# Kernel optimization log

Measured on AMD Instinct MI355X. Metric: run time of the kernel, lower is better.

The kernel has to match this reference:

```python
import jax, jax.numpy as jnp
import numpy as np

B, S, D, H = 4, 2048, 1024, 16
DK = D // H
THETA = 10000.0


def apply_rope(x, pos, theta):
    # x: [B, H, S, DK], pos: [S] int
    d = x.shape[-1]
    inv_freq = theta ** (-jnp.arange(0, d, 2, dtype=jnp.float32) / d)  # [d/2]
    ang = pos.astype(jnp.float32)[:, None] * inv_freq[None, :]          # [S, d/2]
    cos, sin = jnp.cos(ang), jnp.sin(ang)
    x1 = x[..., 0::2]
    x2 = x[..., 1::2]
    r1 = x1 * cos - x2 * sin
    r2 = x1 * sin + x2 * cos
    return jnp.stack([r1, r2], axis=-1).reshape(x.shape)


def setup_inputs() -> dict:
    key = jax.random.key(0)
    ks = jax.random.split(key, 5)
    scale = 1.0 / np.sqrt(D)
    x = jax.random.normal(ks[0], (B, S, D), dtype=jnp.float32)
    Wq = jax.random.normal(ks[1], (D, D), dtype=jnp.float32) * scale
    Wk = jax.random.normal(ks[2], (D, D), dtype=jnp.float32) * scale
    Wv = jax.random.normal(ks[3], (D, D), dtype=jnp.float32) * scale
    Wo = jax.random.normal(ks[4], (D, D), dtype=jnp.float32) * scale
    token_positions = jnp.arange(S, dtype=jnp.int32)
    return {"x": x, "token_positions": token_positions,
            "Wq": Wq, "Wk": Wk, "Wv": Wv, "Wo": Wo}


def reference(x, token_positions, Wq, Wk, Wv, Wo):
    b, s, d = x.shape
    # Linear (no bias), weight stored [out, in]: y = x @ W.T
    q = (x @ Wq.T).reshape(b, s, H, DK).transpose(0, 2, 1, 3)  # [B,H,S,DK]
    k = (x @ Wk.T).reshape(b, s, H, DK).transpose(0, 2, 1, 3)
    v = (x @ Wv.T).reshape(b, s, H, DK).transpose(0, 2, 1, 3)
    q = apply_rope(q, token_positions, THETA)
    k = apply_rope(k, token_positions, THETA)
    scores = jnp.einsum('bhqd,bhkd->bhqk', q, k) / jnp.sqrt(jnp.float32(DK))
    causal = jnp.tril(jnp.ones((s, s), dtype=bool))
    scores = jnp.where(causal, scores, -jnp.inf)
    attn = jax.nn.softmax(scores, axis=-1)
    out = jnp.einsum('bhqk,bhkd->bhqd', attn, v)
    out = out.transpose(0, 2, 1, 3).reshape(b, s, d)
    return out @ Wo.T
```

## Files before the change

### kernel.cpp

```cpp
#include <hip/hip_runtime.h>

typedef unsigned short u16;
typedef __bf16 bf16x8 __attribute__((ext_vector_type(8)));
typedef float f32x4 __attribute__((ext_vector_type(4)));
typedef u16 u16x8 __attribute__((ext_vector_type(8)));
typedef u16 u16x4 __attribute__((ext_vector_type(4)));
typedef short s16x4 __attribute__((ext_vector_type(4)));

union V8 { u16x8 u; bf16x8 b; };
union V4 { u16x4 u; s16x4 s; unsigned w[2]; };

#define NB 4
#define NS 2048
#define ND 1024
#define NH 16
#define NDK 64
#define LP 80
#define CP 136
#define QSCL 0.18033688011112042f
#define FMAX 20.0f

__device__ __forceinline__ u16 f2bf(float f) {
  union { float f; unsigned u; } v; v.f = f;
  return (u16)((v.u + 0x7fffu + ((v.u >> 16) & 1u)) >> 16);
}

__device__ __forceinline__ unsigned pk2bf(float a, float b) {
#if __has_builtin(__builtin_amdgcn_cvt_pk_bf16_f32)
  auto v = __builtin_amdgcn_cvt_pk_bf16_f32(a, b);
  unsigned r; __builtin_memcpy(&r, &v, 4);
  return r;
#else
  return (unsigned)f2bf(a) | ((unsigned)f2bf(b) << 16);
#endif
}

__device__ __forceinline__ float fexp2(float x) {
#if __has_builtin(__builtin_amdgcn_exp2f)
  return __builtin_amdgcn_exp2f(x);
#else
  return exp2f(x);
#endif
}

__device__ __forceinline__ bf16x8 lds_frag(const u16* p) {
  V8 t; t.u = *(const u16x8*)p; return t.b;
}

__global__ __launch_bounds__(256) void cvt_bf16(const float* __restrict__ s,
                                                u16* __restrict__ d, int n) {
  const int i = (blockIdx.x * 256 + threadIdx.x) * 8;
  if (i >= n) return;
  const f32x4 lo = *(const f32x4*)(s + i);
  const f32x4 hi = *(const f32x4*)(s + i + 4);
  union { unsigned w[4]; u16x8 v; } o;
  o.w[0] = pk2bf(lo[0], lo[1]);
  o.w[1] = pk2bf(lo[2], lo[3]);
  o.w[2] = pk2bf(hi[0], hi[1]);
  o.w[3] = pk2bf(hi[2], hi[3]);
  *(u16x8*)(d + i) = o.v;
}

__global__ __launch_bounds__(256) void cvt_w4(const float* __restrict__ w0,
                                              const float* __restrict__ w1,
                                              const float* __restrict__ w2,
                                              const float* __restrict__ w3,
                                              u16* __restrict__ d) {
  const float* s = (blockIdx.y == 0) ? w0 : (blockIdx.y == 1) ? w1
                 : (blockIdx.y == 2) ? w2 : w3;
  const int i = (blockIdx.x * 256 + threadIdx.x) * 8;
  const f32x4 lo = *(const f32x4*)(s + i);
  const f32x4 hi = *(const f32x4*)(s + i + 4);
  union { unsigned w[4]; u16x8 v; } o;
  o.w[0] = pk2bf(lo[0], lo[1]);
  o.w[1] = pk2bf(lo[2], lo[3]);
  o.w[2] = pk2bf(hi[0], hi[1]);
  o.w[3] = pk2bf(hi[2], hi[3]);
  *(u16x8*)(d + (size_t)blockIdx.y * ND * ND + i) = o.v;
}

__global__ __launch_bounds__(256) void gemm_qkv(
    const u16* __restrict__ X, const u16* __restrict__ W0,
    const u16* __restrict__ W1, const u16* __restrict__ W2,
    void* __restrict__ O0, void* __restrict__ O1, void* __restrict__ O2,
    const int* __restrict__ tokpos, int modebase) {
  __shared__ u16 smem[2 * 128 * LP];
  u16* ldsA = smem;
  u16* ldsB = smem + 128 * LP;
  const int tid = threadIdx.x;
  const int lane = tid & 63;
  const int w = tid >> 6;
  const int quad = lane >> 4;
  const int l15 = lane & 15;
  const int z = blockIdx.z;
  const u16* Wp = (z == 0) ? W0 : (z == 1) ? W1 : W2;
  void* Op = (z == 0) ? O0 : (z == 1) ? O1 : O2;
  const int mode = modebase + z;
  const int m0 = blockIdx.x * 128;
  const int n0 = blockIdx.y * 128;
  const int wm = (w >> 1) * 64;
  const int wn = (w & 1) * 64;

  const int srow = tid >> 3;
  const int scol = (tid & 7) * 8;
  const u16* Ag = X + (size_t)(m0 + srow) * ND + scol;
  const u16* Bg = Wp + (size_t)(n0 + srow) * ND + scol;

  f32x4 acc[4][4];
  const f32x4 z4 = {0.f, 0.f, 0.f, 0.f};
  for (int i = 0; i < 4; i++)
    for (int j = 0; j < 4; j++) acc[i][j] = z4;

  for (int k0 = 0; k0 < ND; k0 += 64) {
    u16x8 ar[4], br[4];
    for (int r = 0; r < 4; r++) {
      ar[r] = *(const u16x8*)(Ag + (size_t)r * 32 * ND + k0);
      br[r] = *(const u16x8*)(Bg + (size_t)r * 32 * ND + k0);
    }
    __syncthreads();
    for (int r = 0; r < 4; r++) {
      *(u16x8*)&ldsA[(r * 32 + srow) * LP + scol] = ar[r];
      *(u16x8*)&ldsB[(r * 32 + srow) * LP + scol] = br[r];
    }
    __syncthreads();
    for (int kk = 0; kk < 2; kk++) {
      bf16x8 af[4], bfr[4];
      for (int mt = 0; mt < 4; mt++)
        af[mt] = lds_frag(&ldsA[(wm + mt * 16 + l15) * LP + (kk * 4 + quad) * 8]);
      for (int nt = 0; nt < 4; nt++)
        bfr[nt] = lds_frag(&ldsB[(wn + nt * 16 + l15) * LP + (kk * 4 + quad) * 8]);
      for (int mt = 0; mt < 4; mt++)
        for (int nt = 0; nt < 4; nt++)
          acc[mt][nt] = __builtin_amdgcn_mfma_f32_16x16x32_bf16(
              af[mt], bfr[nt], acc[mt][nt], 0, 0, 0);
    }
  }
  __syncthreads();

  if (mode < 2) {
    u16* cb = smem;
    for (int nt = 0; nt < 4; nt++) {
      const int n_g = n0 + wn + nt * 16 + l15;
      const int dk = n_g & 63;
      const float sgn = (dk & 1) ? 1.f : -1.f;
      const float inv_freq = __expf(-(float)(dk >> 1) * 0.28782313662425572f);
      for (int mt = 0; mt < 4; mt++) {
        const int mrow = wm + mt * 16 + quad * 4;
        for (int r = 0; r < 4; r++) {
          const int m_g = m0 + mrow + r;
          float v = acc[mt][nt][r];
          const int s_i = m_g & (NS - 1);
          const float pos = (float)tokpos[s_i];
          const float partner = __shfl_xor(v, 1);
          float sn, cs;
          __sincosf(pos * inv_freq, &sn, &cs);
          v = v * cs + partner * sn * sgn;
          if (mode == 0) v *= QSCL;
          cb[(mrow + r) * CP + wn + nt * 16 + l15] = f2bf(v);
        }
      }
    }
    __syncthreads();
    const int c = (tid & 15) * 8;
    const int h = (n0 + c) >> 6;
    const int dk0 = (n0 + c) & 63;
    for (int p = 0; p < 8; p++) {
      const int row = p * 16 + (tid >> 4);
      const int m_g = m0 + row;
      const int b = m_g >> 11;
      const int s_i = m_g & (NS - 1);
      *(u16x8*)&((u16*)Op)[(size_t)(((b * NH) + h) * NS + s_i) * NDK + dk0] =
          *(const u16x8*)&cb[row * CP + c];
    }
  } else if (mode == 2) {
    u16* cbT = smem;
    for (int nt = 0; nt < 4; nt++)
      for (int mt = 0; mt < 4; mt++)
        for (int r = 0; r < 4; r++)
          cbT[(wn + nt * 16 + l15) * CP + wm + mt * 16 + quad * 4 + r] =
              f2bf(acc[mt][nt][r]);
    __syncthreads();
    const int b = m0 >> 11;
    const int s0 = m0 & (NS - 1);
    const int col = (tid & 15) * 8;
    for (int p = 0; p < 8; p++) {
      const int row = p * 16 + (tid >> 4);
      const int dkg = n0 + row;
      const int h = dkg >> 6;
      *(u16x8*)&((u16*)Op)[(size_t)(((b * NH) + h) * NDK + (dkg & 63)) * NS +
                           s0 + col] = *(const u16x8*)&cbT[row * CP + col];
    }
  } else {
    for (int nt = 0; nt < 4; nt++) {
      const int n_g = n0 + wn + nt * 16 + l15;
      for (int mt = 0; mt < 4; mt++) {
        const int mb = m0 + wm + mt * 16 + quad * 4;
        for (int r = 0; r < 4; r++)
          ((float*)Op)[(size_t)(mb + r) * ND + n_g] = acc[mt][nt][r];
      }
    }
  }
}

__global__ __launch_bounds__(512, 2) void attn(const u16* __restrict__ Q,
                                               const u16* __restrict__ Kc,
                                               const u16* __restrict__ Vt,
                                               u16* __restrict__ AO,
                                               unsigned* __restrict__ ctr) {
  __shared__ u16 smem[2 * 64 * LP];
  u16* kt = smem;
  u16* vt = smem + 64 * LP;
  __shared__ unsigned s_item;
  const int tid = threadIdx.x;
  const int lane = tid & 63;
  const int w = tid >> 6;
  const int quad = lane >> 4;
  const int l15 = lane & 15;

  if (tid == 0) s_item = atomicAdd(ctr, 1u) & 1023u;
  __syncthreads();
  const unsigned item = s_item;
  const int bh = (int)(item >> 4);
  const int jj = (int)(item & 15u);
  const int qt = (jj & 1) ? (jj >> 1) : (15 - (jj >> 1));
  const int q0 = qt * 128;
  const int qg = q0 + w * 16 + l15;
  const int qmin = q0 + w * 16;

  const u16* Qb = Q + (size_t)bh * NS * NDK + (size_t)qg * NDK + quad * 8;
  const bf16x8 qf0 = lds_frag(Qb);
  const bf16x8 qf1 = lds_frag(Qb + 32);

  int koff[2][4];
#pragma unroll
  for (int kk = 0; kk < 2; kk++)
#pragma unroll
    for (int nt = 0; nt < 4; nt++) {
      const int row = nt * 16 + l15;
      koff[kk][nt] = row * LP + (((kk * 4 + quad) ^ (row & 7)) * 8);
    }
  int voff[4][4];
#pragma unroll
  for (int dt = 0; dt < 4; dt++) {
    const int dk = dt * 16 + l15;
    const int xr = dk & 7;
#pragma unroll
    for (int nt = 0; nt < 4; nt++) {
      const int chunk = 2 * nt + (quad >> 1);
      voff[dt][nt] = dk * LP + ((chunk ^ xr) * 8) + 4 * (quad & 1);
    }
  }

  f32x4 oacc[4];
  const f32x4 z4 = {0.f, 0.f, 0.f, 0.f};
#pragma unroll
  for (int i = 0; i < 4; i++) oacc[i] = z4;
  float ls0 = 0.f, ls1 = 0.f;

  const int srow = tid >> 3;
  const int sg = tid & 7;
  const int woff = srow * LP + ((sg ^ (srow & 7)) * 8);
  const u16* Kb = Kc + (size_t)bh * NS * NDK;
  const u16* Vg = Vt + (size_t)bh * NDK * NS;

  u16x8 kreg = *(const u16x8*)(Kb + (size_t)srow * NDK + sg * 8);
  u16x8 vreg = *(const u16x8*)(Vg + (size_t)srow * NS + sg * 8);

  const int jend = q0 + 64;
  const f32x4 nF = {-FMAX, -FMAX, -FMAX, -FMAX};
  for (int j0 = 0; j0 <= jend; j0 += 64) {
    __syncthreads();
    *(u16x8*)&kt[woff] = kreg;
    *(u16x8*)&vt[woff] = vreg;
    __syncthreads();
    if (j0 + 64 <= jend) {
      const int nj = j0 + 64;
      kreg = *(const u16x8*)(Kb + (size_t)(nj + srow) * NDK + sg * 8);
      vreg = *(const u16x8*)(Vg + (size_t)srow * NS + nj + sg * 8);
    }

    if (j0 <= qmin + 15) {
      f32x4 sa[4];
#pragma unroll
      for (int i = 0; i < 4; i++) sa[i] = nF;
      __builtin_amdgcn_s_setprio(1);
#pragma unroll
      for (int kk = 0; kk < 2; kk++) {
        const bf16x8 qf = kk ? qf1 : qf0;
#pragma unroll
        for (int nt = 0; nt < 4; nt++) {
          const bf16x8 kf = lds_frag(&kt[koff[kk][nt]]);
          sa[nt] = __builtin_amdgcn_mfma_f32_16x16x32_bf16(kf, qf, sa[nt], 0, 0, 0);
        }
      }
      __builtin_amdgcn_s_setprio(0);

      float p[4][4];
#pragma unroll
      for (int nt = 0; nt < 4; nt++)
#pragma unroll
        for (int r = 0; r < 4; r++) p[nt][r] = fexp2(sa[nt][r]);
      if (j0 + 63 > qmin) {
#pragma unroll
        for (int nt = 0; nt < 4; nt++)
#pragma unroll
          for (int r = 0; r < 4; r++)
            if ((j0 + nt * 16 + quad * 4 + r) > qg) p[nt][r] = 0.f;
      }
      {
        float s0 = (p[0][0] + p[0][1]) + (p[0][2] + p[0][3]);
        float s1 = (p[1][0] + p[1][1]) + (p[1][2] + p[1][3]);
        float s2 = (p[2][0] + p[2][1]) + (p[2][2] + p[2][3]);
        float s3 = (p[3][0] + p[3][1]) + (p[3][2] + p[3][3]);
        ls0 += s0 + s1;
        ls1 += s2 + s3;
      }

      s16x4 pa[4];
#pragma unroll
      for (int nt = 0; nt < 4; nt++) {
        V4 t;
        t.w[0] = pk2bf(p[nt][0], p[nt][1]);
        t.w[1] = pk2bf(p[nt][2], p[nt][3]);
        pa[nt] = t.s;
      }

      __builtin_amdgcn_s_setprio(1);
#pragma unroll
      for (int dt = 0; dt < 4; dt++) {
#pragma unroll
        for (int nt = 0; nt < 4; nt++) {
          V4 t;
          t.u = *(const u16x4*)&vt[voff[dt][nt]];
          oacc[dt] = __builtin_amdgcn_mfma_f32_16x16x16bf16_1k(pa[nt], t.s,
                                                               oacc[dt], 0, 0, 0);
        }
      }
      __builtin_amdgcn_s_setprio(0);
    }
  }

  float lsum = ls0 + ls1;
  lsum += __shfl_xor(lsum, 16);
  lsum += __shfl_xor(lsum, 32);
  float lq[4];
#pragma unroll
  for (int r = 0; r < 4; r++) lq[r] = __shfl(lsum, quad * 4 + r);

  __syncthreads();
  u16* ob = smem;
#pragma unroll
  for (int dt = 0; dt < 4; dt++)
#pragma unroll
    for (int r = 0; r < 4; r++)
      ob[(w * 16 + quad * 4 + r) * 72 + dt * 16 + l15] =
          f2bf(oacc[dt][r] / lq[r]);
  __syncthreads();
  const int b = bh >> 4, h = bh & 15;
#pragma unroll
  for (int p2 = 0; p2 < 2; p2++) {
    const int idx = p2 * 512 + tid;
    const int row = idx >> 3;
    const int c = (idx & 7) * 8;
    *(u16x8*)&AO[(size_t)(b * NS + q0 + row) * ND + h * 64 + c] =
        *(const u16x8*)&ob[row * 72 + c];
  }
}

extern "C" void kernel_launch(void* const* d_in, const int* in_sizes, int n_in,
                              void* d_out, int out_size, void* d_ws, size_t ws_size,
                              hipStream_t stream) {
  const float* x = (const float*)d_in[0];
  const int* tp = (const int*)d_in[1];
  const float* Wq = (const float*)d_in[2];
  const float* Wk = (const float*)d_in[3];
  const float* Wv = (const float*)d_in[4];
  const float* Wo = (const float*)d_in[5];

  const size_t NE = (size_t)NB * NS * ND;
  const int NW = ND * ND;
  u16* Qb = (u16*)d_ws;
  u16* Kb = Qb + NE;
  u16* Vtb = Kb + NE;
  u16* Xbf = Vtb + NE;
  u16* Wbf = Xbf + NE;
  unsigned* ctr = (unsigned*)(Wbf + 4 * (size_t)NW);

  dim3 blk(256);
  cvt_bf16<<<dim3((unsigned)(NE / 2048)), blk, 0, stream>>>(x, Xbf, (int)NE);
  cvt_w4<<<dim3(NW / 2048, 4), blk, 0, stream>>>(Wq, Wk, Wv, Wo, Wbf);
  gemm_qkv<<<dim3(64, 8, 3), blk, 0, stream>>>(
      Xbf, Wbf, Wbf + (size_t)NW, Wbf + 2 * (size_t)NW, Qb, Kb, Vtb, tp, 0);
  attn<<<dim3(1024), dim3(512), 0, stream>>>(Qb, Kb, Vtb, Xbf, ctr);
  gemm_qkv<<<dim3(64, 8, 1), blk, 0, stream>>>(
      Xbf, Wbf + 3 * (size_t)NW, Wbf + 3 * (size_t)NW, Wbf + 3 * (size_t)NW,
      d_out, d_out, d_out, tp, 3);
}
```

Before: 284.1 us.

## Precompute RoPE table and restructure attention to load K/V directly from global

Adds a small kernel that precomputes a cos/sin table per position and frequency, so the QKV GEMM epilogue reads the table instead of computing exp and sincos per element. The attention kernel moves from 512 threads to 256 threads per block, with each wave handling 32 query rows as two 16-row fragments. It drops the shared-memory K/V staging and barriers and reads K and V fragments straight from global memory or cache, reusing each K/V fragment across both query fragments. The trade-off is more global or L2 traffic and no software prefetch of K/V, in exchange for fewer synchronisations and more MFMA work per load.

```diff
diff --git a/kernel.cpp b/kernel.cpp
--- a/kernel.cpp
+++ b/kernel.cpp
@@ -79,11 +79,22 @@
   *(u16x8*)(d + (size_t)blockIdx.y * ND * ND + i) = o.v;
 }
 
+__global__ __launch_bounds__(256) void rope_tbl(const int* __restrict__ tp,
+                                                float2* __restrict__ tbl) {
+  const int i = blockIdx.x * 256 + threadIdx.x;
+  const int s = i >> 5, d = i & 31;
+  const float inv = __expf(-(float)d * 0.28782313662425572f);
+  const float ang = (float)tp[s] * inv;
+  float sn, cs;
+  __sincosf(ang, &sn, &cs);
+  tbl[i] = make_float2(cs, sn);
+}
+
 __global__ __launch_bounds__(256) void gemm_qkv(
     const u16* __restrict__ X, const u16* __restrict__ W0,
     const u16* __restrict__ W1, const u16* __restrict__ W2,
     void* __restrict__ O0, void* __restrict__ O1, void* __restrict__ O2,
-    const int* __restrict__ tokpos, int modebase) {
+    const float2* __restrict__ tbl, int modebase) {
   __shared__ u16 smem[2 * 128 * LP];
   u16* ldsA = smem;
   u16* ldsB = smem + 128 * LP;
@@ -143,18 +154,16 @@
       const int n_g = n0 + wn + nt * 16 + l15;
       const int dk = n_g & 63;
       const float sgn = (dk & 1) ? 1.f : -1.f;
-      const float inv_freq = __expf(-(float)(dk >> 1) * 0.28782313662425572f);
+      const int d2 = dk >> 1;
       for (int mt = 0; mt < 4; mt++) {
         const int mrow = wm + mt * 16 + quad * 4;
         for (int r = 0; r < 4; r++) {
           const int m_g = m0 + mrow + r;
           float v = acc[mt][nt][r];
           const int s_i = m_g & (NS - 1);
-          const float pos = (float)tokpos[s_i];
           const float partner = __shfl_xor(v, 1);
-          float sn, cs;
-          __sincosf(pos * inv_freq, &sn, &cs);
-          v = v * cs + partner * sn * sgn;
+          const float2 t = tbl[s_i * 32 + d2];
+          v = v * t.x + partner * t.y * sgn;
           if (mode == 0) v *= QSCL;
           cb[(mrow + r) * CP + wn + nt * 16 + l15] = f2bf(v);
         }
@@ -202,14 +211,12 @@
   }
 }
 
-__global__ __launch_bounds__(512, 2) void attn(const u16* __restrict__ Q,
-                                               const u16* __restrict__ Kc,
-                                               const u16* __restrict__ Vt,
-                                               u16* __restrict__ AO,
-                                               unsigned* __restrict__ ctr) {
-  __shared__ u16 smem[2 * 64 * LP];
-  u16* kt = smem;
-  u16* vt = smem + 64 * LP;
+__global__ __launch_bounds__(256) void attn(const u16* __restrict__ Q,
+                                            const u16* __restrict__ Kc,
+                                            const u16* __restrict__ Vt,
+                                            u16* __restrict__ AO,
+                                            unsigned* __restrict__ ctr) {
+  __shared__ u16 ob[128 * 72];
   __shared__ unsigned s_item;
   const int tid = threadIdx.x;
   const int lane = tid & 63;
@@ -224,142 +231,118 @@
   const int jj = (int)(item & 15u);
   const int qt = (jj & 1) ? (jj >> 1) : (15 - (jj >> 1));
   const int q0 = qt * 128;
-  const int qg = q0 + w * 16 + l15;
-  const int qmin = q0 + w * 16;
-
-  const u16* Qb = Q + (size_t)bh * NS * NDK + (size_t)qg * NDK + quad * 8;
-  const bf16x8 qf0 = lds_frag(Qb);
-  const bf16x8 qf1 = lds_frag(Qb + 32);
-
-  int koff[2][4];
-#pragma unroll
-  for (int kk = 0; kk < 2; kk++)
-#pragma unroll
-    for (int nt = 0; nt < 4; nt++) {
-      const int row = nt * 16 + l15;
-      koff[kk][nt] = row * LP + (((kk * 4 + quad) ^ (row & 7)) * 8);
-    }
-  int voff[4][4];
-#pragma unroll
-  for (int dt = 0; dt < 4; dt++) {
-    const int dk = dt * 16 + l15;
-    const int xr = dk & 7;
-#pragma unroll
-    for (int nt = 0; nt < 4; nt++) {
-      const int chunk = 2 * nt + (quad >> 1);
-      voff[dt][nt] = dk * LP + ((chunk ^ xr) * 8) + 4 * (quad & 1);
-    }
-  }
-
-  f32x4 oacc[4];
+  const int qbase = q0 + w * 32;
+
+  const u16* Qp = Q + (size_t)bh * NS * NDK + (size_t)(qbase + l15) * NDK + quad * 8;
+  bf16x8 qf[2][2];
+  qf[0][0] = lds_frag(Qp);
+  qf[0][1] = lds_frag(Qp + 32);
+  qf[1][0] = lds_frag(Qp + 16 * NDK);
+  qf[1][1] = lds_frag(Qp + 16 * NDK + 32);
+
+  f32x4 oacc[2][4];
   const f32x4 z4 = {0.f, 0.f, 0.f, 0.f};
 #pragma unroll
-  for (int i = 0; i < 4; i++) oacc[i] = z4;
-  float ls0 = 0.f, ls1 = 0.f;
-
-  const int srow = tid >> 3;
-  const int sg = tid & 7;
-  const int woff = srow * LP + ((sg ^ (srow & 7)) * 8);
-  const u16* Kb = Kc + (size_t)bh * NS * NDK;
-  const u16* Vg = Vt + (size_t)bh * NDK * NS;
-
-  u16x8 kreg = *(const u16x8*)(Kb + (size_t)srow * NDK + sg * 8);
-  u16x8 vreg = *(const u16x8*)(Vg + (size_t)srow * NS + sg * 8);
-
-  const int jend = q0 + 64;
+  for (int f = 0; f < 2; f++)
+#pragma unroll
+    for (int i = 0; i < 4; i++) oacc[f][i] = z4;
+  float ls[2] = {0.f, 0.f};
+
+  const u16* Kl = Kc + (size_t)bh * NS * NDK + (size_t)l15 * NDK + quad * 8;
+  const u16* Vl = Vt + (size_t)bh * NDK * NS + (size_t)l15 * NS + quad * 4;
+
+  const int jend = q0 + ((w & 2) ? 64 : 0);
   const f32x4 nF = {-FMAX, -FMAX, -FMAX, -FMAX};
   for (int j0 = 0; j0 <= jend; j0 += 64) {
-    __syncthreads();
-    *(u16x8*)&kt[woff] = kreg;
-    *(u16x8*)&vt[woff] = vreg;
-    __syncthreads();
-    if (j0 + 64 <= jend) {
-      const int nj = j0 + 64;
-      kreg = *(const u16x8*)(Kb + (size_t)(nj + srow) * NDK + sg * 8);
-      vreg = *(const u16x8*)(Vg + (size_t)srow * NS + nj + sg * 8);
-    }
-
-    if (j0 <= qmin + 15) {
-      f32x4 sa[4];
-#pragma unroll
-      for (int i = 0; i < 4; i++) sa[i] = nF;
-      __builtin_amdgcn_s_setprio(1);
-#pragma unroll
-      for (int kk = 0; kk < 2; kk++) {
-        const bf16x8 qf = kk ? qf1 : qf0;
-#pragma unroll
-        for (int nt = 0; nt < 4; nt++) {
-          const bf16x8 kf = lds_frag(&kt[koff[kk][nt]]);
-          sa[nt] = __builtin_amdgcn_mfma_f32_16x16x32_bf16(kf, qf, sa[nt], 0, 0, 0);
+    f32x4 sa[2][4];
+#pragma unroll
+    for (int f = 0; f < 2; f++)
+#pragma unroll
+      for (int i = 0; i < 4; i++) sa[f][i] = nF;
+    __builtin_amdgcn_s_setprio(1);
+#pragma unroll
+    for (int kk = 0; kk < 2; kk++)
+#pragma unroll
+      for (int nt = 0; nt < 4; nt++) {
+        const bf16x8 kf = lds_frag(Kl + (size_t)(j0 + nt * 16) * NDK + kk * 32);
+        sa[0][nt] = __builtin_amdgcn_mfma_f32_16x16x32_bf16(kf, qf[0][kk],
+                                                            sa[0][nt], 0, 0, 0);
+        sa[1][nt] = __builtin_amdgcn_mfma_f32_16x16x32_bf16(kf, qf[1][kk],
+                                                            sa[1][nt], 0, 0, 0);
+      }
+    __builtin_amdgcn_s_setprio(0);
+
+    V4 vf[4][4];
+#pragma unroll
+    for (int dt = 0; dt < 4; dt++)
+#pragma unroll
+      for (int nt = 0; nt < 4; nt++)
+        vf[dt][nt].u = *(const u16x4*)(Vl + (size_t)(dt * 16) * NS + j0 + nt * 16);
+
+    s16x4 pa[2][4];
+#pragma unroll
+    for (int f = 0; f < 2; f++) {
+      const int qgf = qbase + f * 16 + l15;
+      const bool domask = (j0 + 63 > qbase + f * 16);
+      float p[4][4];
+#pragma unroll
+      for (int nt = 0; nt < 4; nt++)
+#pragma unroll
+        for (int r = 0; r < 4; r++) {
+          float e = fexp2(sa[f][nt][r]);
+          if (domask && (j0 + nt * 16 + quad * 4 + r) > qgf) e = 0.f;
+          p[nt][r] = e;
         }
-      }
-      __builtin_amdgcn_s_setprio(0);
-
-      float p[4][4];
-#pragma unroll
-      for (int nt = 0; nt < 4; nt++)
-#pragma unroll
-        for (int r = 0; r < 4; r++) p[nt][r] = fexp2(sa[nt][r]);
-      if (j0 + 63 > qmin) {
-#pragma unroll
-        for (int nt = 0; nt < 4; nt++)
-#pragma unroll
-          for (int r = 0; r < 4; r++)
-            if ((j0 + nt * 16 + quad * 4 + r) > qg) p[nt][r] = 0.f;
-      }
-      {
-        float s0 = (p[0][0] + p[0][1]) + (p[0][2] + p[0][3]);
-        float s1 = (p[1][0] + p[1][1]) + (p[1][2] + p[1][3]);
-        float s2 = (p[2][0] + p[2][1]) + (p[2][2] + p[2][3]);
-        float s3 = (p[3][0] + p[3][1]) + (p[3][2] + p[3][3]);
-        ls0 += s0 + s1;
-        ls1 += s2 + s3;
-      }
-
-      s16x4 pa[4];
+      const float s0 = (p[0][0] + p[0][1]) + (p[0][2] + p[0][3]);
+      const float s1 = (p[1][0] + p[1][1]) + (p[1][2] + p[1][3]);
+      const float s2 = (p[2][0] + p[2][1]) + (p[2][2] + p[2][3]);
+      const float s3 = (p[3][0] + p[3][1]) + (p[3][2] + p[3][3]);
+      ls[f] += (s0 + s1) + (s2 + s3);
 #pragma unroll
       for (int nt = 0; nt < 4; nt++) {
         V4 t;
         t.w[0] = pk2bf(p[nt][0], p[nt][1]);
         t.w[1] = pk2bf(p[nt][2], p[nt][3]);
-        pa[nt] = t.s;
-      }
-
-      __builtin_amdgcn_s_setprio(1);
-#pragma unroll
-      for (int dt = 0; dt < 4; dt++) {
-#pragma unroll
-        for (int nt = 0; nt < 4; nt++) {
-          V4 t;
-          t.u = *(const u16x4*)&vt[voff[dt][nt]];
-          oacc[dt] = __builtin_amdgcn_mfma_f32_16x16x16bf16_1k(pa[nt], t.s,
-                                                               oacc[dt], 0, 0, 0);
-        }
-      }
-      __builtin_amdgcn_s_setprio(0);
-    }
-  }
-
-  float lsum = ls0 + ls1;
-  lsum += __shfl_xor(lsum, 16);
-  lsum += __shfl_xor(lsum, 32);
-  float lq[4];
-#pragma unroll
-  for (int r = 0; r < 4; r++) lq[r] = __shfl(lsum, quad * 4 + r);
-
-  __syncthreads();
-  u16* ob = smem;
-#pragma unroll
-  for (int dt = 0; dt < 4; dt++)
-#pragma unroll
-    for (int r = 0; r < 4; r++)
-      ob[(w * 16 + quad * 4 + r) * 72 + dt * 16 + l15] =
-          f2bf(oacc[dt][r] / lq[r]);
+        pa[f][nt] = t.s;
+      }
+    }
+
+    __builtin_amdgcn_s_setprio(1);
+#pragma unroll
+    for (int dt = 0; dt < 4; dt++)
+#pragma unroll
+      for (int nt = 0; nt < 4; nt++) {
+        oacc[0][dt] = __builtin_amdgcn_mfma_f32_16x16x16bf16_1k(
+            pa[0][nt], vf[dt][nt].s, oacc[0][dt], 0, 0, 0);
+        oacc[1][dt] = __builtin_amdgcn_mfma_f32_16x16x16bf16_1k(
+            pa[1][nt], vf[dt][nt].s, oacc[1][dt], 0, 0, 0);
+      }
+    __builtin_amdgcn_s_setprio(0);
+  }
+
+  float lq[2][4];
+#pragma unroll
+  for (int f = 0; f < 2; f++) {
+    float t = ls[f];
+    t += __shfl_xor(t, 16);
+    t += __shfl_xor(t, 32);
+#pragma unroll
+    for (int r = 0; r < 4; r++) lq[f][r] = __shfl(t, quad * 4 + r);
+  }
+
+#pragma unroll
+  for (int f = 0; f < 2; f++)
+#pragma unroll
+    for (int dt = 0; dt < 4; dt++)
+#pragma unroll
+      for (int r = 0; r < 4; r++)
+        ob[(w * 32 + f * 16 + quad * 4 + r) * 72 + dt * 16 + l15] =
+            f2bf(oacc[f][dt][r] / lq[f][r]);
   __syncthreads();
   const int b = bh >> 4, h = bh & 15;
 #pragma unroll
-  for (int p2 = 0; p2 < 2; p2++) {
-    const int idx = p2 * 512 + tid;
+  for (int p2 = 0; p2 < 4; p2++) {
+    const int idx = p2 * 256 + tid;
     const int row = idx >> 3;
     const int c = (idx & 7) * 8;
     *(u16x8*)&AO[(size_t)(b * NS + q0 + row) * ND + h * 64 + c] =
@@ -384,15 +367,18 @@
   u16* Vtb = Kb + NE;
   u16* Xbf = Vtb + NE;
   u16* Wbf = Xbf + NE;
-  unsigned* ctr = (unsigned*)(Wbf + 4 * (size_t)NW);
+  u16* wend = Wbf + 4 * (size_t)NW;
+  unsigned* ctr = (unsigned*)wend;
+  float2* tbl = (float2*)(wend + 8);
 
   dim3 blk(256);
   cvt_bf16<<<dim3((unsigned)(NE / 2048)), blk, 0, stream>>>(x, Xbf, (int)NE);
   cvt_w4<<<dim3(NW / 2048, 4), blk, 0, stream>>>(Wq, Wk, Wv, Wo, Wbf);
+  rope_tbl<<<dim3(256), blk, 0, stream>>>(tp, tbl);
   gemm_qkv<<<dim3(64, 8, 3), blk, 0, stream>>>(
-      Xbf, Wbf, Wbf + (size_t)NW, Wbf + 2 * (size_t)NW, Qb, Kb, Vtb, tp, 0);
-  attn<<<dim3(1024), dim3(512), 0, stream>>>(Qb, Kb, Vtb, Xbf, ctr);
+      Xbf, Wbf, Wbf + (size_t)NW, Wbf + 2 * (size_t)NW, Qb, Kb, Vtb, tbl, 0);
+  attn<<<dim3(1024), blk, 0, stream>>>(Qb, Kb, Vtb, Xbf, ctr);
   gemm_qkv<<<dim3(64, 8, 1), blk, 0, stream>>>(
       Xbf, Wbf + 3 * (size_t)NW, Wbf + 3 * (size_t)NW, Wbf + 3 * (size_t)NW,
-      d_out, d_out, d_out, tp, 3);
-}
+      d_out, d_out, d_out, tbl, 3);
+}
```

Result: slower. 474.8 us (+67.1%).

## Precompute RoPE table and make attention blocks persistent over two work items

Applied to the files above, without the earlier changes.

Adds a small kernel that builds a cos/sin table per position and frequency, so the QKV GEMM epilogue looks values up instead of evaluating exp and sincos per element. The attention kernel now launches half as many blocks, and each block pulls two work items from the atomic counter. The item order changes to longest query tiles first, interleaved across all batch-heads, aiming for better load balance. This costs an extra launch and table reads, and a block's second item waits until its first is done.

```diff
diff --git a/kernel.cpp b/kernel.cpp
--- a/kernel.cpp
+++ b/kernel.cpp
@@ -79,11 +79,22 @@
   *(u16x8*)(d + (size_t)blockIdx.y * ND * ND + i) = o.v;
 }
 
+__global__ __launch_bounds__(256) void rope_tbl(const int* __restrict__ tp,
+                                                float2* __restrict__ tbl) {
+  const int i = blockIdx.x * 256 + threadIdx.x;
+  const int s = i >> 5, d = i & 31;
+  const float inv = __expf(-(float)d * 0.28782313662425572f);
+  const float ang = (float)tp[s] * inv;
+  float sn, cs;
+  __sincosf(ang, &sn, &cs);
+  tbl[i] = make_float2(cs, sn);
+}
+
 __global__ __launch_bounds__(256) void gemm_qkv(
     const u16* __restrict__ X, const u16* __restrict__ W0,
     const u16* __restrict__ W1, const u16* __restrict__ W2,
     void* __restrict__ O0, void* __restrict__ O1, void* __restrict__ O2,
-    const int* __restrict__ tokpos, int modebase) {
+    const float2* __restrict__ tbl, int modebase) {
   __shared__ u16 smem[2 * 128 * LP];
   u16* ldsA = smem;
   u16* ldsB = smem + 128 * LP;
@@ -143,18 +154,16 @@
       const int n_g = n0 + wn + nt * 16 + l15;
       const int dk = n_g & 63;
       const float sgn = (dk & 1) ? 1.f : -1.f;
-      const float inv_freq = __expf(-(float)(dk >> 1) * 0.28782313662425572f);
+      const int d2 = dk >> 1;
       for (int mt = 0; mt < 4; mt++) {
         const int mrow = wm + mt * 16 + quad * 4;
         for (int r = 0; r < 4; r++) {
           const int m_g = m0 + mrow + r;
           float v = acc[mt][nt][r];
           const int s_i = m_g & (NS - 1);
-          const float pos = (float)tokpos[s_i];
           const float partner = __shfl_xor(v, 1);
-          float sn, cs;
-          __sincosf(pos * inv_freq, &sn, &cs);
-          v = v * cs + partner * sn * sgn;
+          const float2 t = tbl[s_i * 32 + d2];
+          v = v * t.x + partner * t.y * sgn;
           if (mode == 0) v *= QSCL;
           cb[(mrow + r) * CP + wn + nt * 16 + l15] = f2bf(v);
         }
@@ -217,20 +226,6 @@
   const int quad = lane >> 4;
   const int l15 = lane & 15;
 
-  if (tid == 0) s_item = atomicAdd(ctr, 1u) & 1023u;
-  __syncthreads();
-  const unsigned item = s_item;
-  const int bh = (int)(item >> 4);
-  const int jj = (int)(item & 15u);
-  const int qt = (jj & 1) ? (jj >> 1) : (15 - (jj >> 1));
-  const int q0 = qt * 128;
-  const int qg = q0 + w * 16 + l15;
-  const int qmin = q0 + w * 16;
-
-  const u16* Qb = Q + (size_t)bh * NS * NDK + (size_t)qg * NDK + quad * 8;
-  const bf16x8 qf0 = lds_frag(Qb);
-  const bf16x8 qf1 = lds_frag(Qb + 32);
-
   int koff[2][4];
 #pragma unroll
   for (int kk = 0; kk < 2; kk++)
@@ -250,120 +245,136 @@
       voff[dt][nt] = dk * LP + ((chunk ^ xr) * 8) + 4 * (quad & 1);
     }
   }
-
-  f32x4 oacc[4];
-  const f32x4 z4 = {0.f, 0.f, 0.f, 0.f};
-#pragma unroll
-  for (int i = 0; i < 4; i++) oacc[i] = z4;
-  float ls0 = 0.f, ls1 = 0.f;
-
   const int srow = tid >> 3;
   const int sg = tid & 7;
   const int woff = srow * LP + ((sg ^ (srow & 7)) * 8);
-  const u16* Kb = Kc + (size_t)bh * NS * NDK;
-  const u16* Vg = Vt + (size_t)bh * NDK * NS;
-
-  u16x8 kreg = *(const u16x8*)(Kb + (size_t)srow * NDK + sg * 8);
-  u16x8 vreg = *(const u16x8*)(Vg + (size_t)srow * NS + sg * 8);
-
-  const int jend = q0 + 64;
-  const f32x4 nF = {-FMAX, -FMAX, -FMAX, -FMAX};
-  for (int j0 = 0; j0 <= jend; j0 += 64) {
-    __syncthreads();
-    *(u16x8*)&kt[woff] = kreg;
-    *(u16x8*)&vt[woff] = vreg;
-    __syncthreads();
-    if (j0 + 64 <= jend) {
-      const int nj = j0 + 64;
-      kreg = *(const u16x8*)(Kb + (size_t)(nj + srow) * NDK + sg * 8);
-      vreg = *(const u16x8*)(Vg + (size_t)srow * NS + nj + sg * 8);
-    }
-
-    if (j0 <= qmin + 15) {
-      f32x4 sa[4];
-#pragma unroll
-      for (int i = 0; i < 4; i++) sa[i] = nF;
-      __builtin_amdgcn_s_setprio(1);
-#pragma unroll
-      for (int kk = 0; kk < 2; kk++) {
-        const bf16x8 qf = kk ? qf1 : qf0;
-#pragma unroll
-        for (int nt = 0; nt < 4; nt++) {
-          const bf16x8 kf = lds_frag(&kt[koff[kk][nt]]);
-          sa[nt] = __builtin_amdgcn_mfma_f32_16x16x32_bf16(kf, qf, sa[nt], 0, 0, 0);
-        }
+
+  for (int rep = 0; rep < 2; ++rep) {
+    __syncthreads();
+    if (tid == 0) s_item = atomicAdd(ctr, 1u) & 1023u;
+    __syncthreads();
+    const unsigned item = s_item;
+    const int qt = 15 - (int)(item >> 6);
+    const int bh = (int)(item & 63u);
+    const int q0 = qt * 128;
+    const int qg = q0 + w * 16 + l15;
+    const int qmin = q0 + w * 16;
+
+    const u16* Qb = Q + (size_t)bh * NS * NDK + (size_t)qg * NDK + quad * 8;
+    const bf16x8 qf0 = lds_frag(Qb);
+    const bf16x8 qf1 = lds_frag(Qb + 32);
+
+    f32x4 oacc[4];
+    const f32x4 z4 = {0.f, 0.f, 0.f, 0.f};
+#pragma unroll
+    for (int i = 0; i < 4; i++) oacc[i] = z4;
+    float ls0 = 0.f, ls1 = 0.f;
+
+    const u16* Kb = Kc + (size_t)bh * NS * NDK;
+    const u16* Vg = Vt + (size_t)bh * NDK * NS;
+
+    u16x8 kreg = *(const u16x8*)(Kb + (size_t)srow * NDK + sg * 8);
+    u16x8 vreg = *(const u16x8*)(Vg + (size_t)srow * NS + sg * 8);
+
+    const int jend = q0 + 64;
+    const f32x4 nF = {-FMAX, -FMAX, -FMAX, -FMAX};
+    for (int j0 = 0; j0 <= jend; j0 += 64) {
+      __syncthreads();
+      *(u16x8*)&kt[woff] = kreg;
+      *(u16x8*)&vt[woff] = vreg;
+      __syncthreads();
+      if (j0 + 64 <= jend) {
+        const int nj = j0 + 64;
+        kreg = *(const u16x8*)(Kb + (size_t)(nj + srow) * NDK + sg * 8);
+        vreg = *(const u16x8*)(Vg + (size_t)srow * NS + nj + sg * 8);
       }
-      __builtin_amdgcn_s_setprio(0);
-
-      float p[4][4];
-#pragma unroll
-      for (int nt = 0; nt < 4; nt++)
-#pragma unroll
-        for (int r = 0; r < 4; r++) p[nt][r] = fexp2(sa[nt][r]);
-      if (j0 + 63 > qmin) {
+
+      if (j0 <= qmin + 15) {
+        f32x4 sa[4];
+#pragma unroll
+        for (int i = 0; i < 4; i++) sa[i] = nF;
+        __builtin_amdgcn_s_setprio(1);
+#pragma unroll
+        for (int kk = 0; kk < 2; kk++) {
+          const bf16x8 qf = kk ? qf1 : qf0;
+#pragma unroll
+          for (int nt = 0; nt < 4; nt++) {
+            const bf16x8 kf = lds_frag(&kt[koff[kk][nt]]);
+            sa[nt] = __builtin_amdgcn_mfma_f32_16x16x32_bf16(kf, qf, sa[nt], 0, 0, 0);
+          }
+        }
+        __builtin_amdgcn_s_setprio(0);
+
+        float p[4][4];
 #pragma unroll
         for (int nt = 0; nt < 4; nt++)
 #pragma unroll
-          for (int r = 0; r < 4; r++)
-            if ((j0 + nt * 16 + quad * 4 + r) > qg) p[nt][r] = 0.f;
-      }
-      {
-        float s0 = (p[0][0] + p[0][1]) + (p[0][2] + p[0][3]);
-        float s1 = (p[1][0] + p[1][1]) + (p[1][2] + p[1][3]);
-        float s2 = (p[2][0] + p[2][1]) + (p[2][2] + p[2][3]);
-        float s3 = (p[3][0] + p[3][1]) + (p[3][2] + p[3][3]);
-        ls0 += s0 + s1;
-        ls1 += s2 + s3;
-      }
-
-      s16x4 pa[4];
-#pragma unroll
-      for (int nt = 0; nt < 4; nt++) {
-        V4 t;
-        t.w[0] = pk2bf(p[nt][0], p[nt][1]);
-        t.w[1] = pk2bf(p[nt][2], p[nt][3]);
-        pa[nt] = t.s;
-      }
-
-      __builtin_amdgcn_s_setprio(1);
-#pragma unroll
-      for (int dt = 0; dt < 4; dt++) {
+          for (int r = 0; r < 4; r++) p[nt][r] = fexp2(sa[nt][r]);
+        if (j0 + 63 > qmin) {
+#pragma unroll
+          for (int nt = 0; nt < 4; nt++)
+#pragma unroll
+            for (int r = 0; r < 4; r++)
+              if ((j0 + nt * 16 + quad * 4 + r) > qg) p[nt][r] = 0.f;
+        }
+        {
+          float s0 = (p[0][0] + p[0][1]) + (p[0][2] + p[0][3]);
+          float s1 = (p[1][0] + p[1][1]) + (p[1][2] + p[1][3]);
+          float s2 = (p[2][0] + p[2][1]) + (p[2][2] + p[2][3]);
+          float s3 = (p[3][0] + p[3][1]) + (p[3][2] + p[3][3]);
+          ls0 += s0 + s1;
+          ls1 += s2 + s3;
+        }
+
+        s16x4 pa[4];
 #pragma unroll
         for (int nt = 0; nt < 4; nt++) {
           V4 t;
-          t.u = *(const u16x4*)&vt[voff[dt][nt]];
-          oacc[dt] = __builtin_amdgcn_mfma_f32_16x16x16bf16_1k(pa[nt], t.s,
-                                                               oacc[dt], 0, 0, 0);
-        }
+          t.w[0] = pk2bf(p[nt][0], p[nt][1]);
+          t.w[1] = pk2bf(p[nt][2], p[nt][3]);
+          pa[nt] = t.s;
+        }
+
+        __builtin_amdgcn_s_setprio(1);
+#pragma unroll
+        for (int dt = 0; dt < 4; dt++) {
+#pragma unroll
+          for (int nt = 0; nt < 4; nt++) {
+            V4 t;
+            t.u = *(const u16x4*)&vt[voff[dt][nt]];
+            oacc[dt] = __builtin_amdgcn_mfma_f32_16x16x16bf16_1k(pa[nt], t.s,
+                                                                 oacc[dt], 0, 0, 0);
+          }
+        }
+        __builtin_amdgcn_s_setprio(0);
       }
-      __builtin_amdgcn_s_setprio(0);
-    }
-  }
-
-  float lsum = ls0 + ls1;
-  lsum += __shfl_xor(lsum, 16);
-  lsum += __shfl_xor(lsum, 32);
-  float lq[4];
-#pragma unroll
-  for (int r = 0; r < 4; r++) lq[r] = __shfl(lsum, quad * 4 + r);
-
-  __syncthreads();
-  u16* ob = smem;
-#pragma unroll
-  for (int dt = 0; dt < 4; dt++)
-#pragma unroll
-    for (int r = 0; r < 4; r++)
-      ob[(w * 16 + quad * 4 + r) * 72 + dt * 16 + l15] =
-          f2bf(oacc[dt][r] / lq[r]);
-  __syncthreads();
-  const int b = bh >> 4, h = bh & 15;
-#pragma unroll
-  for (int p2 = 0; p2 < 2; p2++) {
-    const int idx = p2 * 512 + tid;
-    const int row = idx >> 3;
-    const int c = (idx & 7) * 8;
-    *(u16x8*)&AO[(size_t)(b * NS + q0 + row) * ND + h * 64 + c] =
-        *(const u16x8*)&ob[row * 72 + c];
+    }
+
+    float lsum = ls0 + ls1;
+    lsum += __shfl_xor(lsum, 16);
+    lsum += __shfl_xor(lsum, 32);
+    float lq[4];
+#pragma unroll
+    for (int r = 0; r < 4; r++) lq[r] = __shfl(lsum, quad * 4 + r);
+
+    __syncthreads();
+    u16* ob = smem;
+#pragma unroll
+    for (int dt = 0; dt < 4; dt++)
+#pragma unroll
+      for (int r = 0; r < 4; r++)
+        ob[(w * 16 + quad * 4 + r) * 72 + dt * 16 + l15] =
+            f2bf(oacc[dt][r] / lq[r]);
+    __syncthreads();
+    const int b = bh >> 4, h = bh & 15;
+#pragma unroll
+    for (int p2 = 0; p2 < 2; p2++) {
+      const int idx = p2 * 512 + tid;
+      const int row = idx >> 3;
+      const int c = (idx & 7) * 8;
+      *(u16x8*)&AO[(size_t)(b * NS + q0 + row) * ND + h * 64 + c] =
+          *(const u16x8*)&ob[row * 72 + c];
+    }
   }
 }
 
@@ -384,15 +395,18 @@
   u16* Vtb = Kb + NE;
   u16* Xbf = Vtb + NE;
   u16* Wbf = Xbf + NE;
-  unsigned* ctr = (unsigned*)(Wbf + 4 * (size_t)NW);
+  u16* wend = Wbf + 4 * (size_t)NW;
+  unsigned* ctr = (unsigned*)wend;
+  float2* tbl = (float2*)(wend + 8);
 
   dim3 blk(256);
   cvt_bf16<<<dim3((unsigned)(NE / 2048)), blk, 0, stream>>>(x, Xbf, (int)NE);
   cvt_w4<<<dim3(NW / 2048, 4), blk, 0, stream>>>(Wq, Wk, Wv, Wo, Wbf);
+  rope_tbl<<<dim3(256), blk, 0, stream>>>(tp, tbl);
   gemm_qkv<<<dim3(64, 8, 3), blk, 0, stream>>>(
-      Xbf, Wbf, Wbf + (size_t)NW, Wbf + 2 * (size_t)NW, Qb, Kb, Vtb, tp, 0);
-  attn<<<dim3(1024), dim3(512), 0, stream>>>(Qb, Kb, Vtb, Xbf, ctr);
+      Xbf, Wbf, Wbf + (size_t)NW, Wbf + 2 * (size_t)NW, Qb, Kb, Vtb, tbl, 0);
+  attn<<<dim3(512), dim3(512), 0, stream>>>(Qb, Kb, Vtb, Xbf, ctr);
   gemm_qkv<<<dim3(64, 8, 1), blk, 0, stream>>>(
       Xbf, Wbf + 3 * (size_t)NW, Wbf + 3 * (size_t)NW, Wbf + 3 * (size_t)NW,
-      d_out, d_out, d_out, tp, 3);
-}
+      d_out, d_out, d_out, tbl, 3);
+}
```

Result: faster. 268.3 us (-5.6%).
